# Kernel tuning notes

Hardware: AMD Instinct MI355X
Metric: run time of the kernel (lower is better)

Reference implementation:

```python
import jax, jax.numpy as jnp
import numpy as np

N_NODES = 100000
N_EDGES = 3200000
IN_CH = 256


def setup_inputs() -> dict:
    key = jax.random.key(0)
    k1, k2, k3 = jax.random.split(key, 3)
    x = jax.random.normal(k1, (N_NODES, IN_CH), dtype=jnp.float32)
    edge_index = jax.random.randint(k2, (2, N_EDGES), 0, N_NODES, dtype=jnp.int64)
    # GCNConv linear: weight [in_channels, 1] (applied as x @ W), bias [1]
    W = jax.random.normal(k3, (IN_CH, 1), dtype=jnp.float32) * (1.0 / np.sqrt(IN_CH))
    b = jnp.zeros((1,), dtype=jnp.float32)
    return {"x": x, "edge_index": edge_index, "W": W, "b": b}


def reference(x, edge_index, W, b):
    # PyG GCNConv(in, 1): h = x @ W; add self-loops; symmetric norm; scatter-add to target; + bias
    N = x.shape[0]
    self_loops = jnp.broadcast_to(jnp.arange(N, dtype=edge_index.dtype)[None, :], (2, N))
    ei = jnp.concatenate([edge_index, self_loops], axis=1)  # [2, E+N]
    src, dst = ei[0], ei[1]

    # degree computed at target (col) with unit edge weights, incl. self-loops
    deg = jax.ops.segment_sum(jnp.ones(ei.shape[1], dtype=x.dtype), dst, num_segments=N)
    deg_inv_sqrt = jnp.where(deg > 0, jax.lax.rsqrt(deg), 0.0)
    norm = deg_inv_sqrt[src] * deg_inv_sqrt[dst]  # [E+N]

    h = x @ W  # [N, 1] — project first (out_channels < in_channels)
    msg = norm[:, None] * h[src]  # [E+N, 1]
    out = jax.ops.segment_sum(msg, dst, num_segments=N)  # [N, 1]
    return out + b
```

## Files before the change

kernel.cpp:

```cpp
#include <hip/hip_runtime.h>

#define GCN_N 100000
#define GCN_E 3200000
#define GCN_C 256

#define BSHIFT 8
#define NBUCK 391
#define BCAP 10240
#define NBP 128
#define NB1 512
#define TB1 1024
#define CHUNK (GCN_E / NB1)
#define PERTHR ((CHUNK + TB1 - 1) / TB1)


__global__ void k_init_cursor(int* __restrict__ cursor) {
    const int p = blockIdx.x * blockDim.x + threadIdx.x;
    if (p < NBUCK) cursor[p] = p * BCAP;
}

__global__ void __launch_bounds__(TB1) k_proj_bin(const float* __restrict__ x,
                                                  const float* __restrict__ W,
                                                  float* __restrict__ h,
                                                  const int* __restrict__ src,
                                                  const int* __restrict__ dst,
                                                  int* __restrict__ cursor,
                                                  int* __restrict__ bpack) {
    __shared__ int hist[NBUCK];
    __shared__ int base[NBUCK];
    __shared__ int lscan[NBUCK];
    __shared__ int wsum[16], woff[16];
    __shared__ int spack[CHUNK];
    __shared__ int sdest[CHUNK];
    const int tid = threadIdx.x;

    if (blockIdx.x < NBP) {
        const int lane = tid & 63;
        const int wave = (blockIdx.x * TB1 + tid) >> 6;
        const int nwaves = NBP * (TB1 / 64);
        const float4 wf = *reinterpret_cast<const float4*>(W + lane * 4);
        for (int i = wave; i < GCN_N; i += nwaves) {
            const float4 xv = *reinterpret_cast<const float4*>(x + (size_t)i * GCN_C + lane * 4);
            float s = xv.x * wf.x + xv.y * wf.y + xv.z * wf.z + xv.w * wf.w;
            #pragma unroll
            for (int off = 32; off > 0; off >>= 1)
                s += __shfl_down(s, off, 64);
            if (lane == 0) h[i] = s;
        }
        return;
    }

    for (int p = tid; p < NBUCK; p += TB1) hist[p] = 0;
    __syncthreads();

    const int c0 = (blockIdx.x - NBP) * CHUNK;
    int my_pack[PERTHR], my_bkt[PERTHR], my_off[PERTHR];
    #pragma unroll
    for (int j = 0; j < PERTHR; ++j) {
        const int k = tid + j * TB1;
        my_bkt[j] = -1;
        if (k < CHUNK) {
            const int d = dst[c0 + k];
            const int s = src[c0 + k];
            const int b = d >> BSHIFT;
            my_pack[j] = (s << BSHIFT) | (d & 255);
            my_bkt[j]  = b;
            my_off[j]  = atomicAdd(&hist[b], 1);
        }
    }
    __syncthreads();

    if (tid < NBUCK) base[tid] = atomicAdd(&cursor[tid], hist[tid]);
    {
        const int lane = tid & 63, w = tid >> 6;
        int v = (tid < NBUCK) ? hist[tid] : 0;
        #pragma unroll
        for (int d2 = 1; d2 < 64; d2 <<= 1) {
            const int t = __shfl_up(v, d2, 64);
            if (lane >= d2) v += t;
        }
        if (lane == 63) wsum[w] = v;
        __syncthreads();
        if (tid < 16) {
            int s = 0;
            for (int k = 0; k < tid; ++k) s += wsum[k];
            woff[tid] = s;
        }
        __syncthreads();
        if (tid < NBUCK) lscan[tid] = v + woff[w];
    }
    __syncthreads();

    #pragma unroll
    for (int j = 0; j < PERTHR; ++j) {
        if (my_bkt[j] >= 0) {
            const int b    = my_bkt[j];
            const int slot = lscan[b] - hist[b] + my_off[j];
            const int gpos = base[b] + my_off[j];
            spack[slot] = my_pack[j];
            sdest[slot] = (gpos < (b + 1) * BCAP) ? gpos : -1;
        }
    }
    __syncthreads();

    for (int i = tid; i < CHUNK; i += TB1) {
        const int dpos = sdest[i];
        if (dpos >= 0) bpack[dpos] = spack[i];
    }
}

__global__ void __launch_bounds__(1024) k_deg_norm(const int* __restrict__ bpack,
                                                   const int* __restrict__ cursor,
                                                   const float* __restrict__ h,
                                                   float* __restrict__ dis,
                                                   float* __restrict__ g) {
    __shared__ int cnt[256];
    const int p = blockIdx.x, tid = threadIdx.x;
    if (tid < 256) cnt[tid] = 0;
    __syncthreads();
    const int s0 = p * BCAP;
    const int s1 = min(cursor[p], (p + 1) * BCAP);
    for (int i = s0 + tid; i < s1; i += 1024)
        atomicAdd(&cnt[bpack[i] & 255], 1);
    __syncthreads();
    if (tid < 256) {
        const int node = (p << BSHIFT) + tid;
        if (node < GCN_N) {
            const float r = rsqrtf(1.0f + (float)cnt[tid]);
            dis[node] = r;
            g[node]   = r * h[node];
        }
    }
}

__global__ void __launch_bounds__(1024) k_scatter_bin(const int* __restrict__ bpack,
                                                      const int* __restrict__ cursor,
                                                      const float* __restrict__ g,
                                                      const float* __restrict__ dis,
                                                      const float* __restrict__ bias,
                                                      float* __restrict__ out) {
    __shared__ float acc[256];
    const int p = blockIdx.x, tid = threadIdx.x;
    if (tid < 256) acc[tid] = 0.0f;
    __syncthreads();
    const int s0 = p * BCAP;
    const int s1 = min(cursor[p], (p + 1) * BCAP);
    for (int i = s0 + tid; i < s1; i += 1024) {
        const int pk = bpack[i];
        atomicAdd(&acc[pk & 255], g[pk >> BSHIFT]);
    }
    __syncthreads();
    if (tid < 256) {
        const int node = (p << BSHIFT) + tid;
        if (node < GCN_N)
            out[node] = bias[0] + dis[node] * (acc[tid] + g[node]);
    }
}


__global__ void k_zero(float* __restrict__ a, int n) {
    int i = blockIdx.x * blockDim.x + threadIdx.x;
    const int stride = gridDim.x * blockDim.x;
    for (; i < n; i += stride) a[i] = 0.0f;
}
__global__ void k_proj_sep(const float* __restrict__ x, const float* __restrict__ W,
                           float* __restrict__ h, int n) {
    const int lane   = threadIdx.x & 63;
    const int wave   = (blockIdx.x * blockDim.x + threadIdx.x) >> 6;
    const int nwaves = (gridDim.x * blockDim.x) >> 6;
    const float4 wf = *reinterpret_cast<const float4*>(W + lane * 4);
    for (int i = wave; i < n; i += nwaves) {
        const float4 xv = *reinterpret_cast<const float4*>(x + (size_t)i * GCN_C + lane * 4);
        float s = xv.x * wf.x + xv.y * wf.y + xv.z * wf.z + xv.w * wf.w;
        #pragma unroll
        for (int off = 32; off > 0; off >>= 1)
            s += __shfl_down(s, off, 64);
        if (lane == 0) h[i] = s;
    }
}
__global__ void k_degree_flat(const int* __restrict__ dst, float* __restrict__ deg, int e) {
    int i = blockIdx.x * blockDim.x + threadIdx.x;
    const int stride = gridDim.x * blockDim.x;
    for (; i < e; i += stride) atomicAdd(&deg[dst[i]], 1.0f);
}
__global__ void k_norm_flat(const float* __restrict__ h, float* __restrict__ deg_dis,
                            float* __restrict__ out, const float* __restrict__ bias, int n) {
    const int i = blockIdx.x * blockDim.x + threadIdx.x;
    if (i < n) {
        const float r = rsqrtf(deg_dis[i] + 1.0f);
        deg_dis[i] = r;
        out[i] = bias[0] + r * r * h[i];
    }
}
__global__ void k_scatter_flat(const int* __restrict__ src, const int* __restrict__ dst,
                               const float* __restrict__ h, const float* __restrict__ dis,
                               float* __restrict__ out, int e) {
    int i = blockIdx.x * blockDim.x + threadIdx.x;
    const int stride = gridDim.x * blockDim.x;
    for (; i < e; i += stride) {
        const int s = src[i], d = dst[i];
        atomicAdd(&out[d], dis[s] * dis[d] * h[s]);
    }
}

extern "C" void kernel_launch(void* const* d_in, const int* in_sizes, int n_in,
                              void* d_out, int out_size, void* d_ws, size_t ws_size,
                              hipStream_t stream) {
    const float* x  = (const float*)d_in[0];
    const int*   ei = (const int*)d_in[1];
    const float* W  = (const float*)d_in[2];
    const float* b  = (const float*)d_in[3];
    float* out = (float*)d_out;

    const int* src = ei;
    const int* dst = ei + GCN_E;

    const size_t need_bin = ((size_t)3 * GCN_N + NBUCK + (size_t)NBUCK * BCAP) * sizeof(float);
    if (ws_size >= need_bin) {
        float* h      = (float*)d_ws;
        float* dis    = h + GCN_N;
        float* g      = dis + GCN_N;
        int*   cursor = (int*)(g + GCN_N);
        int*   bpack  = cursor + NBUCK;

        k_init_cursor<<<(NBUCK + 255) / 256, 256, 0, stream>>>(cursor);
        k_proj_bin<<<NBP + NB1, TB1, 0, stream>>>(x, W, h, src, dst, cursor, bpack);
        k_deg_norm<<<NBUCK, 1024, 0, stream>>>(bpack, cursor, h, dis, g);
        k_scatter_bin<<<NBUCK, 1024, 0, stream>>>(bpack, cursor, g, dis, b, out);
    } else {
        float* h   = (float*)d_ws;
        float* deg = h + GCN_N;
        k_zero<<<512, 256, 0, stream>>>(deg, GCN_N);
        k_proj_sep<<<2048, 256, 0, stream>>>(x, W, h, GCN_N);
        k_degree_flat<<<2048, 256, 0, stream>>>(dst, deg, GCN_E);
        k_norm_flat<<<(GCN_N + 255) / 256, 256, 0, stream>>>(h, deg, out, b, GCN_N);
        k_scatter_flat<<<2048, 256, 0, stream>>>(src, dst, h, deg, out, GCN_E);
    }
}
```

Before: 74.12 us.

## Replace global atomic bucket cursors with per-block histogram, scan, and deterministic placement

Splits edge binning into three passes. A histogram kernel (fused with the projection) counts per-block bucket sizes, a column scan over blocks computes exact offsets, and a placement kernel writes packed edges into buckets. This removes the global atomic cursor contention and the cursor-init launch, and makes bucket order deterministic. The cost is reading dst twice, an extra launch, and a per-block count matrix in workspace. Block sizes, bucket capacity and a 4-row unrolled projection are also retuned.

```diff
diff --git a/kernel.cpp b/kernel.cpp
--- a/kernel.cpp
+++ b/kernel.cpp
@@ -6,111 +6,157 @@
 
 #define BSHIFT 8
 #define NBUCK 391
-#define BCAP 10240
-#define NBP 128
-#define NB1 512
-#define TB1 1024
-#define CHUNK (GCN_E / NB1)
-#define PERTHR ((CHUNK + TB1 - 1) / TB1)
-
-
-__global__ void k_init_cursor(int* __restrict__ cursor) {
-    const int p = blockIdx.x * blockDim.x + threadIdx.x;
-    if (p < NBUCK) cursor[p] = p * BCAP;
-}
-
-__global__ void __launch_bounds__(TB1) k_proj_bin(const float* __restrict__ x,
+#define BCAP 9216
+#define NBP 512
+#define NB4 1024
+#define CHUNK (GCN_E / NB4)
+#define TB 512
+#define PERTHR ((CHUNK + TB - 1) / TB)
+
+__global__ void __launch_bounds__(TB) k_proj_hist(const float* __restrict__ x,
                                                   const float* __restrict__ W,
                                                   float* __restrict__ h,
-                                                  const int* __restrict__ src,
                                                   const int* __restrict__ dst,
-                                                  int* __restrict__ cursor,
-                                                  int* __restrict__ bpack) {
+                                                  int* __restrict__ cnts) {
     __shared__ int hist[NBUCK];
-    __shared__ int base[NBUCK];
+    const int tid = threadIdx.x;
+
+    if (blockIdx.x < NBP) {
+        const int lane   = tid & 63;
+        const int wave   = (blockIdx.x * TB + tid) >> 6;
+        const int nwaves = NBP * (TB / 64);
+        const float4 wf = *reinterpret_cast<const float4*>(W + lane * 4);
+        for (int i = wave * 4; i < GCN_N; i += nwaves * 4) {
+            const float4 a0 = *reinterpret_cast<const float4*>(x + (size_t)(i + 0) * GCN_C + lane * 4);
+            const float4 a1 = *reinterpret_cast<const float4*>(x + (size_t)(i + 1) * GCN_C + lane * 4);
+            const float4 a2 = *reinterpret_cast<const float4*>(x + (size_t)(i + 2) * GCN_C + lane * 4);
+            const float4 a3 = *reinterpret_cast<const float4*>(x + (size_t)(i + 3) * GCN_C + lane * 4);
+            float s0 = a0.x * wf.x + a0.y * wf.y + a0.z * wf.z + a0.w * wf.w;
+            float s1 = a1.x * wf.x + a1.y * wf.y + a1.z * wf.z + a1.w * wf.w;
+            float s2 = a2.x * wf.x + a2.y * wf.y + a2.z * wf.z + a2.w * wf.w;
+            float s3 = a3.x * wf.x + a3.y * wf.y + a3.z * wf.z + a3.w * wf.w;
+            #pragma unroll
+            for (int off = 32; off > 0; off >>= 1) {
+                s0 += __shfl_down(s0, off, 64);
+                s1 += __shfl_down(s1, off, 64);
+                s2 += __shfl_down(s2, off, 64);
+                s3 += __shfl_down(s3, off, 64);
+            }
+            if (lane == 0) {
+                h[i + 0] = s0; h[i + 1] = s1; h[i + 2] = s2; h[i + 3] = s3;
+            }
+        }
+        return;
+    }
+
+    const int blk = blockIdx.x - NBP;
+    for (int b = tid; b < NBUCK; b += TB) hist[b] = 0;
+    __syncthreads();
+    const int c0 = blk * CHUNK;
+    for (int k = tid; k < CHUNK; k += TB)
+        atomicAdd(&hist[dst[c0 + k] >> BSHIFT], 1);
+    __syncthreads();
+    for (int b = tid; b < NBUCK; b += TB)
+        cnts[(size_t)blk * NBUCK + b] = hist[b];
+}
+
+__global__ void __launch_bounds__(1024) k_scan(int* __restrict__ cb, int* __restrict__ fill) {
+    __shared__ int wsum[16], woff[16];
+    const int b = blockIdx.x, tid = threadIdx.x;
+    const int lane = tid & 63, w = tid >> 6;
+    const int v = cb[(size_t)tid * NBUCK + b];
+    int incl = v;
+    #pragma unroll
+    for (int d = 1; d < 64; d <<= 1) {
+        const int t = __shfl_up(incl, d, 64);
+        if (lane >= d) incl += t;
+    }
+    if (lane == 63) wsum[w] = incl;
+    __syncthreads();
+    if (tid == 0) {
+        int s = 0;
+        #pragma unroll
+        for (int k = 0; k < 16; ++k) { woff[k] = s; s += wsum[k]; }
+    }
+    __syncthreads();
+    const int excl = incl - v + woff[w];
+    cb[(size_t)tid * NBUCK + b] = b * BCAP + excl;
+    if (tid == 1023) fill[b] = min(excl + v, BCAP);
+}
+
+__global__ void __launch_bounds__(TB) k_place(const int* __restrict__ src,
+                                              const int* __restrict__ dst,
+                                              const int* __restrict__ bases,
+                                              int* __restrict__ bpack) {
+    __shared__ int hist[NBUCK];
     __shared__ int lscan[NBUCK];
-    __shared__ int wsum[16], woff[16];
+    __shared__ int base_s[NBUCK];
+    __shared__ int wsum[8], woff[8];
     __shared__ int spack[CHUNK];
     __shared__ int sdest[CHUNK];
-    const int tid = threadIdx.x;
-
-    if (blockIdx.x < NBP) {
-        const int lane = tid & 63;
-        const int wave = (blockIdx.x * TB1 + tid) >> 6;
-        const int nwaves = NBP * (TB1 / 64);
-        const float4 wf = *reinterpret_cast<const float4*>(W + lane * 4);
-        for (int i = wave; i < GCN_N; i += nwaves) {
-            const float4 xv = *reinterpret_cast<const float4*>(x + (size_t)i * GCN_C + lane * 4);
-            float s = xv.x * wf.x + xv.y * wf.y + xv.z * wf.z + xv.w * wf.w;
-            #pragma unroll
-            for (int off = 32; off > 0; off >>= 1)
-                s += __shfl_down(s, off, 64);
-            if (lane == 0) h[i] = s;
-        }
-        return;
-    }
-
-    for (int p = tid; p < NBUCK; p += TB1) hist[p] = 0;
-    __syncthreads();
-
-    const int c0 = (blockIdx.x - NBP) * CHUNK;
-    int my_pack[PERTHR], my_bkt[PERTHR], my_off[PERTHR];
+    const int tid = threadIdx.x, blk = blockIdx.x;
+
+    for (int b = tid; b < NBUCK; b += TB) {
+        hist[b]   = 0;
+        base_s[b] = bases[(size_t)blk * NBUCK + b];
+    }
+    __syncthreads();
+
+    const int c0 = blk * CHUNK;
+    int my_off[PERTHR];
     #pragma unroll
     for (int j = 0; j < PERTHR; ++j) {
-        const int k = tid + j * TB1;
-        my_bkt[j] = -1;
+        const int k = tid + j * TB;
+        if (k < CHUNK)
+            my_off[j] = atomicAdd(&hist[dst[c0 + k] >> BSHIFT], 1);
+    }
+    __syncthreads();
+
+    {
+        int v = (tid < NBUCK) ? hist[tid] : 0;
+        const int lane = tid & 63, w = tid >> 6;
+        int incl = v;
+        #pragma unroll
+        for (int d = 1; d < 64; d <<= 1) {
+            const int t = __shfl_up(incl, d, 64);
+            if (lane >= d) incl += t;
+        }
+        if (lane == 63) wsum[w] = incl;
+        __syncthreads();
+        if (tid == 0) {
+            int s = 0;
+            #pragma unroll
+            for (int k = 0; k < 8; ++k) { woff[k] = s; s += wsum[k]; }
+        }
+        __syncthreads();
+        if (tid < NBUCK) lscan[tid] = incl - v + woff[w];
+    }
+    __syncthreads();
+
+    #pragma unroll
+    for (int j = 0; j < PERTHR; ++j) {
+        const int k = tid + j * TB;
         if (k < CHUNK) {
             const int d = dst[c0 + k];
             const int s = src[c0 + k];
             const int b = d >> BSHIFT;
-            my_pack[j] = (s << BSHIFT) | (d & 255);
-            my_bkt[j]  = b;
-            my_off[j]  = atomicAdd(&hist[b], 1);
-        }
-    }
-    __syncthreads();
-
-    if (tid < NBUCK) base[tid] = atomicAdd(&cursor[tid], hist[tid]);
-    {
-        const int lane = tid & 63, w = tid >> 6;
-        int v = (tid < NBUCK) ? hist[tid] : 0;
-        #pragma unroll
-        for (int d2 = 1; d2 < 64; d2 <<= 1) {
-            const int t = __shfl_up(v, d2, 64);
-            if (lane >= d2) v += t;
-        }
-        if (lane == 63) wsum[w] = v;
-        __syncthreads();
-        if (tid < 16) {
-            int s = 0;
-            for (int k = 0; k < tid; ++k) s += wsum[k];
-            woff[tid] = s;
-        }
-        __syncthreads();
-        if (tid < NBUCK) lscan[tid] = v + woff[w];
-    }
-    __syncthreads();
-
-    #pragma unroll
-    for (int j = 0; j < PERTHR; ++j) {
-        if (my_bkt[j] >= 0) {
-            const int b    = my_bkt[j];
-            const int slot = lscan[b] - hist[b] + my_off[j];
-            const int gpos = base[b] + my_off[j];
-            spack[slot] = my_pack[j];
+            const int off  = my_off[j];
+            const int slot = lscan[b] + off;
+            const int gpos = base_s[b] + off;
+            spack[slot] = (s << BSHIFT) | (d & 255);
             sdest[slot] = (gpos < (b + 1) * BCAP) ? gpos : -1;
         }
     }
     __syncthreads();
 
-    for (int i = tid; i < CHUNK; i += TB1) {
+    for (int i = tid; i < CHUNK; i += TB) {
         const int dpos = sdest[i];
         if (dpos >= 0) bpack[dpos] = spack[i];
     }
 }
 
 __global__ void __launch_bounds__(1024) k_deg_norm(const int* __restrict__ bpack,
-                                                   const int* __restrict__ cursor,
+                                                   const int* __restrict__ fill,
                                                    const float* __restrict__ h,
                                                    float* __restrict__ dis,
                                                    float* __restrict__ g) {
@@ -118,8 +164,7 @@
     const int p = blockIdx.x, tid = threadIdx.x;
     if (tid < 256) cnt[tid] = 0;
     __syncthreads();
-    const int s0 = p * BCAP;
-    const int s1 = min(cursor[p], (p + 1) * BCAP);
+    const int s0 = p * BCAP, s1 = s0 + fill[p];
     for (int i = s0 + tid; i < s1; i += 1024)
         atomicAdd(&cnt[bpack[i] & 255], 1);
     __syncthreads();
@@ -134,7 +179,7 @@
 }
 
 __global__ void __launch_bounds__(1024) k_scatter_bin(const int* __restrict__ bpack,
-                                                      const int* __restrict__ cursor,
+                                                      const int* __restrict__ fill,
                                                       const float* __restrict__ g,
                                                       const float* __restrict__ dis,
                                                       const float* __restrict__ bias,
@@ -143,8 +188,7 @@
     const int p = blockIdx.x, tid = threadIdx.x;
     if (tid < 256) acc[tid] = 0.0f;
     __syncthreads();
-    const int s0 = p * BCAP;
-    const int s1 = min(cursor[p], (p + 1) * BCAP);
+    const int s0 = p * BCAP, s1 = s0 + fill[p];
     for (int i = s0 + tid; i < s1; i += 1024) {
         const int pk = bpack[i];
         atomicAdd(&acc[pk & 255], g[pk >> BSHIFT]);
@@ -215,18 +259,22 @@
     const int* src = ei;
     const int* dst = ei + GCN_E;
 
-    const size_t need_bin = ((size_t)3 * GCN_N + NBUCK + (size_t)NBUCK * BCAP) * sizeof(float);
-    if (ws_size >= need_bin) {
-        float* h      = (float*)d_ws;
-        float* dis    = h + GCN_N;
-        float* g      = dis + GCN_N;
-        int*   cursor = (int*)(g + GCN_N);
-        int*   bpack  = cursor + NBUCK;
-
-        k_init_cursor<<<(NBUCK + 255) / 256, 256, 0, stream>>>(cursor);
-        k_proj_bin<<<NBP + NB1, TB1, 0, stream>>>(x, W, h, src, dst, cursor, bpack);
-        k_deg_norm<<<NBUCK, 1024, 0, stream>>>(bpack, cursor, h, dis, g);
-        k_scatter_bin<<<NBUCK, 1024, 0, stream>>>(bpack, cursor, g, dis, b, out);
+    const size_t need = ((size_t)3 * GCN_N + NBUCK
+                         + (size_t)NB4 * NBUCK
+                         + (size_t)NBUCK * BCAP) * 4;
+    if (ws_size >= need) {
+        float* h    = (float*)d_ws;
+        float* dis  = h + GCN_N;
+        float* g    = dis + GCN_N;
+        int*   fill = (int*)(g + GCN_N);
+        int*   cb   = fill + NBUCK;
+        int*   bpack = cb + (size_t)NB4 * NBUCK;
+
+        k_proj_hist<<<NBP + NB4, TB, 0, stream>>>(x, W, h, dst, cb);
+        k_scan<<<NBUCK, 1024, 0, stream>>>(cb, fill);
+        k_place<<<NB4, TB, 0, stream>>>(src, dst, cb, bpack);
+        k_deg_norm<<<NBUCK, 1024, 0, stream>>>(bpack, fill, h, dis, g);
+        k_scatter_bin<<<NBUCK, 1024, 0, stream>>>(bpack, fill, g, dis, b, out);
     } else {
         float* h   = (float*)d_ws;
         float* deg = h + GCN_N;
```

After: 73.14 us. No clear change (-1.3%).
